# Optimization experiments

Hardware: AMD Instinct MI355X
Metric: run time of the kernel (lower is better)

The kernel has to match this reference:

```python
import jax, jax.numpy as jnp
import numpy as np

N, E = 50000, 400000
EMB, IN, HID, HEADS = 128, 128, 128, 3
RRELU_SLOPE = (1.0 / 8.0 + 1.0 / 3.0) / 2.0  # torch.rrelu eval-mode slope


def _gat_conv(h_in, src, dst, W, a_src, a_dst, b, concat):
    """PyG-style GATConv. h_in: [N, F_in]; src/dst: [E'] (self-loops included)."""
    n = h_in.shape[0]
    h = (h_in @ W).reshape(n, HEADS, -1)            # [N, H, C]
    e_src = jnp.sum(h * a_src, axis=-1)             # [N, H]
    e_dst = jnp.sum(h * a_dst, axis=-1)             # [N, H]
    e = jax.nn.leaky_relu(e_src[src] + e_dst[dst], 0.2)  # [E', H]
    # softmax over incoming edges of each target node
    m = jax.ops.segment_max(e, dst, num_segments=n)
    ex = jnp.exp(e - m[dst])
    denom = jax.ops.segment_sum(ex, dst, num_segments=n)
    alpha = ex / denom[dst]                          # [E', H]
    out = jax.ops.segment_sum(h[src] * alpha[:, :, None], dst, num_segments=n)  # [N,H,C]
    out = out.reshape(n, -1) if concat else out.mean(axis=1)
    return out + b


def _rrelu(x):
    return jnp.where(x >= 0, x, x * RRELU_SLOPE)


def setup_inputs() -> dict:
    key = jax.random.key(0)
    ks = jax.random.split(key, 16)
    d_in = IN + EMB

    def glorot(k, shape):
        fan = sum(shape)
        return jax.random.normal(k, shape, jnp.float32) * np.sqrt(2.0 / fan)

    return {
        "z": jax.random.normal(ks[0], (N, EMB), jnp.float32),
        "x": jax.random.normal(ks[1], (N, IN), jnp.float32),
        "ei": jax.random.randint(ks[2], (2, E), 0, N, jnp.int32),
        "W1": glorot(ks[3], (d_in, HEADS * HID)),
        "a1_src": glorot(ks[4], (HEADS, HID)),
        "a1_dst": glorot(ks[5], (HEADS, HID)),
        "b1": jnp.zeros((HID,), jnp.float32),                 # concat=False -> size C
        "W2": glorot(ks[6], (HID, HEADS * HID)),
        "a2_src": glorot(ks[7], (HEADS, HID)),
        "a2_dst": glorot(ks[8], (HEADS, HID)),
        "b2": jnp.zeros((HEADS * HID,), jnp.float32),         # concat=True -> size H*C
        "W_lin": glorot(ks[9], (HEADS * HID, 1)),
        "b_lin": jnp.zeros((1,), jnp.float32),
    }


def reference(z, x, ei, W1, a1_src, a1_dst, b1, W2, a2_src, a2_dst, b2, W_lin, b_lin):
    n = x.shape[0]
    loops = jnp.arange(n, dtype=ei.dtype)
    src = jnp.concatenate([ei[0], loops])  # PyG add_self_loops=True
    dst = jnp.concatenate([ei[1], loops])
    h = jnp.concatenate([z, x], axis=1)
    h = _rrelu(_gat_conv(h, src, dst, W1, a1_src, a1_dst, b1, concat=False))
    h = _rrelu(_gat_conv(h, src, dst, W2, a2_src, a2_dst, b2, concat=True))
    return jax.nn.sigmoid(h @ W_lin + b_lin)
```

## Files before the change

kernel.cpp:

```cpp
#include <hip/hip_runtime.h>
#include <stdint.h>

#define HEADS 3
#define HID 128
#define FDIM (HEADS * HID)

typedef __attribute__((ext_vector_type(8))) short bf16x8;
typedef __attribute__((ext_vector_type(4))) float f32x4;

__device__ __forceinline__ float lrelu(float x) { return x >= 0.f ? x : 0.2f * x; }
__device__ __forceinline__ float rrelu(float x) {
    const float SLOPE = (1.0f / 8.0f + 1.0f / 3.0f) * 0.5f;
    return x >= 0.f ? x : SLOPE * x;
}
__device__ __forceinline__ unsigned short f2bf(float f) {
    union { float f; unsigned u; } c; c.f = f;
    unsigned r = c.u + 0x7FFF + ((c.u >> 16) & 1);
    return (unsigned short)(r >> 16);
}
__device__ __forceinline__ float bflo(unsigned u) {
    union { unsigned u; float f; } c; c.u = u << 16; return c.f;
}
__device__ __forceinline__ float bfhi(unsigned u) {
    union { unsigned u; float f; } c; c.u = u & 0xffff0000u; return c.f;
}

__device__ __forceinline__ void gload_lds16(const void* g, void* l) {
    __builtin_amdgcn_global_load_lds(
        (const __attribute__((address_space(1))) void*)g,
        (__attribute__((address_space(3))) void*)l, 16, 0, 0);
}


__global__ void k_hist(const int* __restrict__ dst, int E, int* __restrict__ cnt) {
    for (int i = blockIdx.x * blockDim.x + threadIdx.x; i < E; i += gridDim.x * blockDim.x)
        atomicAdd(&cnt[dst[i]], 1);
}

#define SC_T 256
#define SC_E 8
#define SC_CHUNK (SC_T * SC_E)

__global__ __launch_bounds__(SC_T) void k_scan1(const int* __restrict__ cnt,
                                                int* __restrict__ exc,
                                                int* __restrict__ bsum, int n) {
    __shared__ int sm[SC_T];
    int b = blockIdx.x, t = threadIdx.x;
    int base = b * SC_CHUNK + t * SC_E;
    int v[SC_E];
    int s = 0;
#pragma unroll
    for (int i = 0; i < SC_E; i++) {
        int idx = base + i;
        v[i] = (idx < n) ? cnt[idx] : 0;
        s += v[i];
    }
    sm[t] = s;
    __syncthreads();
    for (int off = 1; off < SC_T; off <<= 1) {
        int x = (t >= off) ? sm[t - off] : 0;
        __syncthreads();
        sm[t] += x;
        __syncthreads();
    }
    int run = sm[t] - s;
    if (t == SC_T - 1) bsum[b] = sm[t];
#pragma unroll
    for (int i = 0; i < SC_E; i++) {
        int idx = base + i;
        if (idx < n) exc[idx] = run;
        run += v[i];
    }
}

__global__ __launch_bounds__(256) void k_scan2(const int* __restrict__ bsum,
                                               int* __restrict__ bpre, int nb) {
    __shared__ int sm[256];
    int t = threadIdx.x;
    int v = (t < nb) ? bsum[t] : 0;
    sm[t] = v;
    __syncthreads();
    for (int off = 1; off < 256; off <<= 1) {
        int x = (t >= off) ? sm[t - off] : 0;
        __syncthreads();
        sm[t] += x;
        __syncthreads();
    }
    if (t < nb) bpre[t + 1] = sm[t];
    if (t == 0) bpre[0] = 0;
}

__global__ void k_scan3(int* __restrict__ offs, const int* __restrict__ bpre,
                        int* __restrict__ cursor, int n, int nb) {
    int i = blockIdx.x * blockDim.x + threadIdx.x;
    if (i < n) {
        int o = offs[i] + bpre[i / SC_CHUNK];
        offs[i] = o;
        cursor[i] = o;
    }
    if (i == 0) offs[n] = bpre[nb];
}

__global__ void k_scatter(const int* __restrict__ src, const int* __restrict__ dst, int E,
                          int* __restrict__ cursor, int* __restrict__ ssrc,
                          int* __restrict__ sdst) {
    for (int i = blockIdx.x * blockDim.x + threadIdx.x; i < E; i += gridDim.x * blockDim.x) {
        int d = dst[i];
        int p = atomicAdd(&cursor[d], 1);
        ssrc[p] = src[i];
        sdst[p] = d;
    }
}


__global__ void k_cvt_wt(const float* __restrict__ W, unsigned short* __restrict__ WT,
                         int K, int Ncols) {
    int n = blockIdx.x;
    for (int k = threadIdx.x; k < K; k += blockDim.x)
        WT[(size_t)n * K + k] = f2bf(W[(size_t)k * Ncols + n]);
}


template <bool F32A>
__global__ __launch_bounds__(256) void k_gemm(
    const void* __restrict__ Ap0, const void* __restrict__ Ap1, int Nn,
    const unsigned short* __restrict__ BT,
    unsigned short* __restrict__ C,
    int K, int Ncols,
    const float* __restrict__ asrc, const float* __restrict__ adst,
    float* __restrict__ es, float* __restrict__ ed, int Nnodes) {
    __shared__ __align__(16) unsigned short As[64 * 32];
    __shared__ __align__(16) unsigned short Bs[128 * 32];
    __shared__ float esP[64][2], edP[64][2];
    int tid = threadIdx.x;
    int w = tid >> 6, lane = tid & 63;
    int row0 = blockIdx.x * 64;
    int head = blockIdx.y;
    int col0 = head * 128;
    int wr = w >> 1, wc = w & 1;

    f32x4 acc[2][4] = {};
    int frow = lane & 15;
    int fk = (lane >> 4) * 8;

    const float* zf = (const float*)Ap0;
    const float* xf = (const float*)Ap1;
    float4 va[2];
    if (F32A) {
#pragma unroll
        for (int i = 0; i < 2; i++) {
            int idx = i * 256 + tid;
            int row = idx >> 3, c4 = (idx & 7) * 4;
            int gr = row0 + row;
            const float* sp = zf + (size_t)gr * 128 + c4;
            va[i] = (gr < Nn) ? *(const float4*)sp : make_float4(0.f, 0.f, 0.f, 0.f);
        }
    }

    for (int k0 = 0; k0 < K; k0 += 32) {
#pragma unroll
        for (int i = 0; i < 2; i++) {
            int c = (i * 4 + w) * 64 + lane;
            gload_lds16(BT + (size_t)(col0 + (c >> 2)) * K + k0 + (c & 3) * 8,
                        (char*)Bs + (i * 4 + w) * 1024);
        }
        if (F32A) {
#pragma unroll
            for (int i = 0; i < 2; i++) {
                int idx = i * 256 + tid;
                unsigned short o[4] = {f2bf(va[i].x), f2bf(va[i].y),
                                       f2bf(va[i].z), f2bf(va[i].w)};
                *(uint2*)((char*)As + (size_t)idx * 8) = *(uint2*)o;
            }
        } else {
            const unsigned short* A = (const unsigned short*)Ap0;
            int c = tid;
            gload_lds16(A + (size_t)(row0 + (c >> 2)) * K + k0 + (c & 3) * 8,
                        (char*)As + w * 1024);
        }
        asm volatile("s_waitcnt vmcnt(0)" ::: "memory");
        __syncthreads();

        if (F32A && (k0 + 32 < K)) {
            int kn = k0 + 32;
#pragma unroll
            for (int i = 0; i < 2; i++) {
                int idx = i * 256 + tid;
                int row = idx >> 3, c4 = (idx & 7) * 4;
                int gr = row0 + row;
                const float* sp = (kn < 128)
                                      ? (zf + (size_t)gr * 128 + kn + c4)
                                      : (xf + (size_t)gr * 128 + (kn - 128) + c4);
                va[i] = (gr < Nn) ? *(const float4*)sp : make_float4(0.f, 0.f, 0.f, 0.f);
            }
        }

        bf16x8 af[2], bfr[4];
#pragma unroll
        for (int m = 0; m < 2; m++)
            af[m] = *(const bf16x8*)&As[(wr * 32 + m * 16 + frow) * 32 + fk];
#pragma unroll
        for (int n = 0; n < 4; n++)
            bfr[n] = *(const bf16x8*)&Bs[(wc * 64 + n * 16 + frow) * 32 + fk];
#pragma unroll
        for (int m = 0; m < 2; m++)
#pragma unroll
            for (int n = 0; n < 4; n++)
                acc[m][n] = __builtin_amdgcn_mfma_f32_16x16x32_bf16(af[m], bfr[n], acc[m][n], 0, 0, 0);
        __syncthreads();
    }

    int ccol = lane & 15, crow = (lane >> 4) * 4;

#pragma unroll
    for (int m = 0; m < 2; m++)
#pragma unroll
        for (int n = 0; n < 4; n++)
#pragma unroll
            for (int j = 0; j < 4; j++) {
                int r = row0 + wr * 32 + m * 16 + crow + j;
                int cc = col0 + wc * 64 + n * 16 + ccol;
                C[(size_t)r * Ncols + cc] = f2bf(acc[m][n][j]);
            }

    float as4[4], ad4[4];
#pragma unroll
    for (int n = 0; n < 4; n++) {
        int col_sub = wc * 64 + n * 16 + ccol;
        as4[n] = asrc[head * HID + col_sub];
        ad4[n] = adst[head * HID + col_sub];
    }
#pragma unroll
    for (int m = 0; m < 2; m++)
#pragma unroll
        for (int j = 0; j < 4; j++) {
            float ps = 0.f, pd = 0.f;
#pragma unroll
            for (int n = 0; n < 4; n++) {
                float v = acc[m][n][j];
                ps = fmaf(v, as4[n], ps);
                pd = fmaf(v, ad4[n], pd);
            }
#pragma unroll
            for (int off = 1; off < 16; off <<= 1) {
                ps += __shfl_xor(ps, off);
                pd += __shfl_xor(pd, off);
            }
            if (ccol == 0) {
                int row_sub = wr * 32 + m * 16 + crow + j;
                esP[row_sub][wc] = ps;
                edP[row_sub][wc] = pd;
            }
        }
    __syncthreads();
    if (tid < 64) {
        int r = row0 + tid;
        if (r < Nnodes) {
            es[(size_t)r * 4 + head] = esP[tid][0] + esP[tid][1];
            ed[(size_t)r * 4 + head] = edP[tid][0] + edP[tid][1];
        }
    }
}


__global__ void k_edge_w(const int* __restrict__ ssrc, const int* __restrict__ sdst,
                         const float* __restrict__ es, const float* __restrict__ ed,
                         float4* __restrict__ w4, int E) {
    for (int j = blockIdx.x * blockDim.x + threadIdx.x; j < E; j += gridDim.x * blockDim.x) {
        int s = ssrc[j], d = sdst[j];
        float4 a = *(const float4*)&es[(size_t)s * 4];
        float4 b = *(const float4*)&ed[(size_t)d * 4];
        float w0 = __expf(lrelu(a.x + b.x));
        float w1 = __expf(lrelu(a.y + b.y));
        float w2 = __expf(lrelu(a.z + b.z));
        w4[j] = make_float4(w0, w1, w2, 0.f);
    }
}


#define EDGE_UNROLL4(body)                                                       \
    int j = j0;                                                                  \
    for (; j + 4 <= j1; j += 4) {                                                \
        int si[4]; float4 wv[4]; unsigned uu[4][3];                              \
        _Pragma("unroll") for (int e = 0; e < 4; e++) si[e] = ssrc[j + e];       \
        _Pragma("unroll") for (int e = 0; e < 4; e++) wv[e] = w4[j + e];         \
        _Pragma("unroll") for (int e = 0; e < 4; e++) {                          \
            const unsigned* rp = Hu + (size_t)si[e] * 192 + L;                   \
            uu[e][0] = rp[0]; uu[e][1] = rp[64]; uu[e][2] = rp[128];             \
        }                                                                        \
        _Pragma("unroll") for (int e = 0; e < 4; e++) { body(wv[e], uu[e]) }     \
    }                                                                            \
    for (; j < j1; j++) {                                                        \
        int s1_ = ssrc[j]; float4 w_ = w4[j];                                    \
        const unsigned* rp = Hu + (size_t)s1_ * 192 + L;                         \
        unsigned u_[3] = {rp[0], rp[64], rp[128]};                               \
        { body(w_, u_) }                                                         \
    }

#define ACC3(wv, uv)                                                             \
    a0[0] = fmaf(wv.x, bflo(uv[0]), a0[0]); a1[0] = fmaf(wv.x, bfhi(uv[0]), a1[0]); \
    a0[1] = fmaf(wv.y, bflo(uv[1]), a0[1]); a1[1] = fmaf(wv.y, bfhi(uv[1]), a1[1]); \
    a0[2] = fmaf(wv.z, bflo(uv[2]), a0[2]); a1[2] = fmaf(wv.z, bfhi(uv[2]), a1[2]); \
    den0 += wv.x; den1 += wv.y; den2 += wv.z;

__global__ __launch_bounds__(256) void k_agg_mean(const unsigned* __restrict__ Hu,
                                                  const float4* __restrict__ w4,
                                                  const float* __restrict__ es,
                                                  const float* __restrict__ ed,
                                                  const int* __restrict__ offs,
                                                  const int* __restrict__ ssrc,
                                                  const float* __restrict__ b,
                                                  unsigned* __restrict__ out, int Nn) {
    int L = threadIdx.x & 63;
    int wstep = gridDim.x * 4;
    for (int n = blockIdx.x * 4 + (threadIdx.x >> 6); n < Nn; n += wstep) {
        float4 esn = *(const float4*)&es[(size_t)n * 4];
        float4 edn = *(const float4*)&ed[(size_t)n * 4];
        float s0 = __expf(lrelu(esn.x + edn.x));
        float s1 = __expf(lrelu(esn.y + edn.y));
        float s2 = __expf(lrelu(esn.z + edn.z));
        float den0 = s0, den1 = s1, den2 = s2;
        const unsigned* rp = Hu + (size_t)n * 192 + L;
        unsigned u0 = rp[0], u1 = rp[64], u2 = rp[128];
        float a0[3] = {s0 * bflo(u0), s1 * bflo(u1), s2 * bflo(u2)};
        float a1[3] = {s0 * bfhi(u0), s1 * bfhi(u1), s2 * bfhi(u2)};
        int j0 = offs[n], j1 = offs[n + 1];
        EDGE_UNROLL4(ACC3)
        float iv0 = 1.f / den0, iv1 = 1.f / den1, iv2 = 1.f / den2;
        int c0 = 2 * L;
        float2 bb = *(const float2*)&b[c0];
        float m0 = (a0[0] * iv0 + a0[1] * iv1 + a0[2] * iv2) * (1.f / 3.f) + bb.x;
        float m1 = (a1[0] * iv0 + a1[1] * iv1 + a1[2] * iv2) * (1.f / 3.f) + bb.y;
        unsigned short o[2] = {f2bf(rrelu(m0)), f2bf(rrelu(m1))};
        out[(size_t)n * 64 + L] = *(unsigned*)o;
    }
}

__global__ __launch_bounds__(256) void k_agg_cat_final(const unsigned* __restrict__ Hu,
                                                       const float4* __restrict__ w4,
                                                       const float* __restrict__ es,
                                                       const float* __restrict__ ed,
                                                       const int* __restrict__ offs,
                                                       const int* __restrict__ ssrc,
                                                       const float* __restrict__ b,
                                                       const float* __restrict__ Wl,
                                                       const float* __restrict__ bl,
                                                       float* __restrict__ out, int Nn) {
    int L = threadIdx.x & 63;
    int wstep = gridDim.x * 4;
    for (int n = blockIdx.x * 4 + (threadIdx.x >> 6); n < Nn; n += wstep) {
        float4 esn = *(const float4*)&es[(size_t)n * 4];
        float4 edn = *(const float4*)&ed[(size_t)n * 4];
        float s0 = __expf(lrelu(esn.x + edn.x));
        float s1 = __expf(lrelu(esn.y + edn.y));
        float s2 = __expf(lrelu(esn.z + edn.z));
        float den0 = s0, den1 = s1, den2 = s2;
        const unsigned* rp = Hu + (size_t)n * 192 + L;
        unsigned u0 = rp[0], u1 = rp[64], u2 = rp[128];
        float a0[3] = {s0 * bflo(u0), s1 * bflo(u1), s2 * bflo(u2)};
        float a1[3] = {s0 * bfhi(u0), s1 * bfhi(u1), s2 * bfhi(u2)};
        int j0 = offs[n], j1 = offs[n + 1];
        EDGE_UNROLL4(ACC3)
        float ivv[3] = {1.f / den0, 1.f / den1, 1.f / den2};
        float p = 0.f;
#pragma unroll
        for (int k = 0; k < 3; k++) {
            int col = k * HID + 2 * L;
            float2 bb = *(const float2*)&b[col];
            float2 wl = *(const float2*)&Wl[col];
            float r0 = rrelu(a0[k] * ivv[k] + bb.x);
            float r1 = rrelu(a1[k] * ivv[k] + bb.y);
            p = fmaf(r0, wl.x, p);
            p = fmaf(r1, wl.y, p);
        }
#pragma unroll
        for (int off = 32; off > 0; off >>= 1) p += __shfl_down(p, off);
        if (L == 0) out[n] = 1.f / (1.f + __expf(-(p + bl[0])));
    }
}


extern "C" void kernel_launch(void* const* d_in, const int* in_sizes, int n_in,
                              void* d_out, int out_size, void* d_ws, size_t ws_size,
                              hipStream_t stream) {
    const float* z   = (const float*)d_in[0];
    const float* x   = (const float*)d_in[1];
    const int*   ei  = (const int*)d_in[2];
    const float* W1  = (const float*)d_in[3];
    const float* a1s = (const float*)d_in[4];
    const float* a1d = (const float*)d_in[5];
    const float* b1  = (const float*)d_in[6];
    const float* W2  = (const float*)d_in[7];
    const float* a2s = (const float*)d_in[8];
    const float* a2d = (const float*)d_in[9];
    const float* b2  = (const float*)d_in[10];
    const float* Wl  = (const float*)d_in[11];
    const float* bl  = (const float*)d_in[12];
    float* outp = (float*)d_out;

    int Nn = in_sizes[0] / 128;
    int E  = in_sizes[2] / 2;
    int Mpad = (Nn + 127) & ~127;
    int nb = (Nn + SC_CHUNK - 1) / SC_CHUNK;

    char* p = (char*)d_ws;
    auto carve = [&](size_t bytes) -> char* {
        char* r = p;
        p += (bytes + 255) & ~(size_t)255;
        return r;
    };
    int*            offs   = (int*)carve((size_t)(Nn + 1) * 4);
    int*            cursor = (int*)carve((size_t)Nn * 4);
    int*            ssrc   = (int*)carve((size_t)E * 4);
    int*            sdst   = (int*)carve((size_t)E * 4);
    int*            bsum   = (int*)carve((size_t)(nb + 1) * 4);
    int*            bpre   = (int*)carve((size_t)(nb + 1) * 4);
    float*          e1s    = (float*)carve((size_t)Mpad * 16);
    float*          e1d    = (float*)carve((size_t)Mpad * 16);
    float4*         w4     = (float4*)carve((size_t)E * 16);
    unsigned short* W1T    = (unsigned short*)carve((size_t)FDIM * 256 * 2);
    unsigned short* W2T    = (unsigned short*)carve((size_t)FDIM * 128 * 2);
    unsigned short* Hbf    = (unsigned short*)carve((size_t)Mpad * FDIM * 2);
    unsigned short* H2in   = (unsigned short*)carve((size_t)Mpad * 128 * 2);

    const int* srcI = ei;
    const int* dstI = ei + E;

    hipMemsetAsync(cursor, 0, (size_t)Nn * 4, stream);
    k_hist<<<1024, 256, 0, stream>>>(dstI, E, cursor);
    k_scan1<<<nb, SC_T, 0, stream>>>(cursor, offs, bsum, Nn);
    k_scan2<<<1, 256, 0, stream>>>(bsum, bpre, nb);
    k_scan3<<<(Nn + 255) / 256, 256, 0, stream>>>(offs, bpre, cursor, Nn, nb);
    k_scatter<<<1024, 256, 0, stream>>>(srcI, dstI, E, cursor, ssrc, sdst);

    k_cvt_wt<<<FDIM, 256, 0, stream>>>(W1, W1T, 256, FDIM);
    k_cvt_wt<<<FDIM, 128, 0, stream>>>(W2, W2T, 128, FDIM);
    hipMemsetAsync(H2in + (size_t)Nn * 128, 0, (size_t)(Mpad - Nn) * 128 * 2, stream);

    dim3 gg(Mpad / 64, FDIM / 128);

    k_gemm<true><<<gg, 256, 0, stream>>>(z, x, Nn, W1T, Hbf, 256, FDIM,
                                         a1s, a1d, e1s, e1d, Nn);
    k_edge_w<<<1024, 256, 0, stream>>>(ssrc, sdst, e1s, e1d, w4, E);
    k_agg_mean<<<2048, 256, 0, stream>>>((const unsigned*)Hbf, w4, e1s, e1d, offs,
                                         ssrc, b1, (unsigned*)H2in, Nn);

    k_gemm<false><<<gg, 256, 0, stream>>>(H2in, nullptr, Mpad, W2T, Hbf, 128, FDIM,
                                          a2s, a2d, e1s, e1d, Nn);
    k_edge_w<<<1024, 256, 0, stream>>>(ssrc, sdst, e1s, e1d, w4, E);
    k_agg_cat_final<<<2048, 256, 0, stream>>>((const unsigned*)Hbf, w4, e1s, e1d, offs,
                                              ssrc, b2, Wl, bl, outp, Nn);
}
```

Baseline: 250.3 us.

## Keep full A row-tile in LDS and loop all heads per block with double-buffered B

The GEMM now loads the whole 64-row A tile, converting it to bf16 and padding its rows, into LDS once, then loops over all three heads inside one block instead of launching one block per head. Re-reading and re-converting the fp32 z/x inputs three times is avoided. B tiles are double-buffered so the next slice's load overlaps current MFMA work, and the two weight-transpose launches are merged into one. In exchange, LDS use per block grows (about 34KB for K=256), the grid shrinks threefold, and each block runs a longer serial loop, which may lower occupancy and parallelism.

```diff
diff --git a/kernel.cpp b/kernel.cpp
--- a/kernel.cpp
+++ b/kernel.cpp
@@ -113,11 +113,17 @@
 }
 
 
-__global__ void k_cvt_wt(const float* __restrict__ W, unsigned short* __restrict__ WT,
-                         int K, int Ncols) {
-    int n = blockIdx.x;
-    for (int k = threadIdx.x; k < K; k += blockDim.x)
-        WT[(size_t)n * K + k] = f2bf(W[(size_t)k * Ncols + n]);
+__global__ void k_cvt_wt2(const float* __restrict__ W1, unsigned short* __restrict__ W1T,
+                          const float* __restrict__ W2, unsigned short* __restrict__ W2T) {
+    int b = blockIdx.x;
+    if (b < FDIM) {
+        for (int k = threadIdx.x; k < 256; k += blockDim.x)
+            W1T[(size_t)b * 256 + k] = f2bf(W1[(size_t)k * FDIM + b]);
+    } else {
+        int n = b - FDIM;
+        for (int k = threadIdx.x; k < 128; k += blockDim.x)
+            W2T[(size_t)n * 128 + k] = f2bf(W2[(size_t)k * FDIM + n]);
+    }
 }
 
 
@@ -129,137 +135,151 @@
     int K, int Ncols,
     const float* __restrict__ asrc, const float* __restrict__ adst,
     float* __restrict__ es, float* __restrict__ ed, int Nnodes) {
-    __shared__ __align__(16) unsigned short As[64 * 32];
-    __shared__ __align__(16) unsigned short Bs[128 * 32];
+    __shared__ __align__(16) unsigned short As[64 * 264];
+    __shared__ __align__(16) unsigned short Bs[2][128 * 32];
     __shared__ float esP[64][2], edP[64][2];
     int tid = threadIdx.x;
     int w = tid >> 6, lane = tid & 63;
     int row0 = blockIdx.x * 64;
-    int head = blockIdx.y;
-    int col0 = head * 128;
     int wr = w >> 1, wc = w & 1;
-
-    f32x4 acc[2][4] = {};
+    int KP = K + 8;
+    int KS = K >> 5;
+
     int frow = lane & 15;
     int fk = (lane >> 4) * 8;
 
-    const float* zf = (const float*)Ap0;
-    const float* xf = (const float*)Ap1;
-    float4 va[2];
     if (F32A) {
-#pragma unroll
-        for (int i = 0; i < 2; i++) {
+        const float* zf = (const float*)Ap0;
+        const float* xf = (const float*)Ap1;
+#pragma unroll 8
+        for (int i = 0; i < 16; i++) {
             int idx = i * 256 + tid;
-            int row = idx >> 3, c4 = (idx & 7) * 4;
+            int row = idx >> 6;
+            int c4 = (idx & 63) * 4;
             int gr = row0 + row;
-            const float* sp = zf + (size_t)gr * 128 + c4;
-            va[i] = (gr < Nn) ? *(const float4*)sp : make_float4(0.f, 0.f, 0.f, 0.f);
+            float4 v = make_float4(0.f, 0.f, 0.f, 0.f);
+            if (gr < Nn) {
+                const float* sp = (c4 < 128) ? zf + (size_t)gr * 128 + c4
+                                             : xf + (size_t)gr * 128 + (c4 - 128);
+                v = *(const float4*)sp;
+            }
+            unsigned short o[4] = {f2bf(v.x), f2bf(v.y), f2bf(v.z), f2bf(v.w)};
+            *(uint2*)&As[row * KP + c4] = *(uint2*)o;
         }
-    }
-
-    for (int k0 = 0; k0 < K; k0 += 32) {
-#pragma unroll
-        for (int i = 0; i < 2; i++) {
-            int c = (i * 4 + w) * 64 + lane;
-            gload_lds16(BT + (size_t)(col0 + (c >> 2)) * K + k0 + (c & 3) * 8,
-                        (char*)Bs + (i * 4 + w) * 1024);
+    } else {
+        const unsigned short* A = (const unsigned short*)Ap0;
+        int cpr = K >> 3;
+#pragma unroll 4
+        for (int i = 0; i < 4; i++) {
+            int idx = i * 256 + tid;
+            int row = idx / cpr;
+            int c8 = (idx - row * cpr) * 8;
+            uint4 v = *(const uint4*)&A[(size_t)(row0 + row) * K + c8];
+            *(uint4*)&As[row * KP + c8] = v;
         }
-        if (F32A) {
-#pragma unroll
-            for (int i = 0; i < 2; i++) {
-                int idx = i * 256 + tid;
-                unsigned short o[4] = {f2bf(va[i].x), f2bf(va[i].y),
-                                       f2bf(va[i].z), f2bf(va[i].w)};
-                *(uint2*)((char*)As + (size_t)idx * 8) = *(uint2*)o;
-            }
-        } else {
-            const unsigned short* A = (const unsigned short*)Ap0;
-            int c = tid;
-            gload_lds16(A + (size_t)(row0 + (c >> 2)) * K + k0 + (c & 3) * 8,
-                        (char*)As + w * 1024);
-        }
+    }
+
+#define STAGE_B(hh, kk, buf)                                                      \
+    {                                                                             \
+        int k0s = (kk) << 5;                                                      \
+        _Pragma("unroll") for (int i = 0; i < 2; i++) {                           \
+            int c = (i * 4 + w) * 64 + lane;                                      \
+            gload_lds16(BT + (size_t)((hh) * 128 + (c >> 2)) * K + k0s + (c & 3) * 8, \
+                        (char*)Bs[buf] + (i * 4 + w) * 1024);                     \
+        }                                                                         \
+    }
+
+    STAGE_B(0, 0, 0)
+
+    f32x4 acc[2][4] = {};
+    int cur = 0;
+    int h = 0, ks = 0;
+    int total = 3 * KS;
+    for (int it = 0; it < total; ++it) {
         asm volatile("s_waitcnt vmcnt(0)" ::: "memory");
         __syncthreads();
 
-        if (F32A && (k0 + 32 < K)) {
-            int kn = k0 + 32;
-#pragma unroll
-            for (int i = 0; i < 2; i++) {
-                int idx = i * 256 + tid;
-                int row = idx >> 3, c4 = (idx & 7) * 4;
-                int gr = row0 + row;
-                const float* sp = (kn < 128)
-                                      ? (zf + (size_t)gr * 128 + kn + c4)
-                                      : (xf + (size_t)gr * 128 + (kn - 128) + c4);
-                va[i] = (gr < Nn) ? *(const float4*)sp : make_float4(0.f, 0.f, 0.f, 0.f);
-            }
-        }
-
+        int nh = h, nks = ks + 1;
+        if (nks == KS) { nh = h + 1; nks = 0; }
+        if (nh < 3) STAGE_B(nh, nks, cur ^ 1)
+
+        int k0 = ks << 5;
         bf16x8 af[2], bfr[4];
 #pragma unroll
         for (int m = 0; m < 2; m++)
-            af[m] = *(const bf16x8*)&As[(wr * 32 + m * 16 + frow) * 32 + fk];
+            af[m] = *(const bf16x8*)&As[(wr * 32 + m * 16 + frow) * KP + k0 + fk];
 #pragma unroll
         for (int n = 0; n < 4; n++)
-            bfr[n] = *(const bf16x8*)&Bs[(wc * 64 + n * 16 + frow) * 32 + fk];
+            bfr[n] = *(const bf16x8*)&Bs[cur][(wc * 64 + n * 16 + frow) * 32 + fk];
 #pragma unroll
         for (int m = 0; m < 2; m++)
 #pragma unroll
             for (int n = 0; n < 4; n++)
                 acc[m][n] = __builtin_amdgcn_mfma_f32_16x16x32_bf16(af[m], bfr[n], acc[m][n], 0, 0, 0);
-        __syncthreads();
-    }
-
-    int ccol = lane & 15, crow = (lane >> 4) * 4;
-
-#pragma unroll
-    for (int m = 0; m < 2; m++)
-#pragma unroll
-        for (int n = 0; n < 4; n++)
-#pragma unroll
-            for (int j = 0; j < 4; j++) {
-                int r = row0 + wr * 32 + m * 16 + crow + j;
-                int cc = col0 + wc * 64 + n * 16 + ccol;
-                C[(size_t)r * Ncols + cc] = f2bf(acc[m][n][j]);
+
+        if (ks == KS - 1) {
+            int ccol = lane & 15, crow = (lane >> 4) * 4;
+            int col0 = h * 128;
+#pragma unroll
+            for (int m = 0; m < 2; m++)
+#pragma unroll
+                for (int n = 0; n < 4; n++)
+#pragma unroll
+                    for (int j = 0; j < 4; j++) {
+                        int r = row0 + wr * 32 + m * 16 + crow + j;
+                        int cc = col0 + wc * 64 + n * 16 + ccol;
+                        C[(size_t)r * Ncols + cc] = f2bf(acc[m][n][j]);
+                    }
+            float as4[4], ad4[4];
+#pragma unroll
+            for (int n = 0; n < 4; n++) {
+                int col_sub = wc * 64 + n * 16 + ccol;
+                as4[n] = asrc[h * HID + col_sub];
+                ad4[n] = adst[h * HID + col_sub];
             }
-
-    float as4[4], ad4[4];
-#pragma unroll
-    for (int n = 0; n < 4; n++) {
-        int col_sub = wc * 64 + n * 16 + ccol;
-        as4[n] = asrc[head * HID + col_sub];
-        ad4[n] = adst[head * HID + col_sub];
-    }
-#pragma unroll
-    for (int m = 0; m < 2; m++)
-#pragma unroll
-        for (int j = 0; j < 4; j++) {
-            float ps = 0.f, pd = 0.f;
-#pragma unroll
-            for (int n = 0; n < 4; n++) {
-                float v = acc[m][n][j];
-                ps = fmaf(v, as4[n], ps);
-                pd = fmaf(v, ad4[n], pd);
+#pragma unroll
+            for (int m = 0; m < 2; m++)
+#pragma unroll
+                for (int j = 0; j < 4; j++) {
+                    float ps = 0.f, pd = 0.f;
+#pragma unroll
+                    for (int n = 0; n < 4; n++) {
+                        float v = acc[m][n][j];
+                        ps = fmaf(v, as4[n], ps);
+                        pd = fmaf(v, ad4[n], pd);
+                    }
+#pragma unroll
+                    for (int off = 1; off < 16; off <<= 1) {
+                        ps += __shfl_xor(ps, off);
+                        pd += __shfl_xor(pd, off);
+                    }
+                    if (ccol == 0) {
+                        int row_sub = wr * 32 + m * 16 + crow + j;
+                        esP[row_sub][wc] = ps;
+                        edP[row_sub][wc] = pd;
+                    }
+                }
+            __syncthreads();
+            if (tid < 64) {
+                int r = row0 + tid;
+                if (r < Nnodes) {
+                    es[(size_t)r * 4 + h] = esP[tid][0] + esP[tid][1];
+                    ed[(size_t)r * 4 + h] = edP[tid][0] + edP[tid][1];
+                }
             }
 #pragma unroll
-            for (int off = 1; off < 16; off <<= 1) {
-                ps += __shfl_xor(ps, off);
-                pd += __shfl_xor(pd, off);
-            }
-            if (ccol == 0) {
-                int row_sub = wr * 32 + m * 16 + crow + j;
-                esP[row_sub][wc] = ps;
-                edP[row_sub][wc] = pd;
-            }
+            for (int m = 0; m < 2; m++)
+#pragma unroll
+                for (int n = 0; n < 4; n++)
+                    acc[m][n] = f32x4{0.f, 0.f, 0.f, 0.f};
+            h++;
+            ks = 0;
+        } else {
+            ks++;
         }
-    __syncthreads();
-    if (tid < 64) {
-        int r = row0 + tid;
-        if (r < Nnodes) {
-            es[(size_t)r * 4 + head] = esP[tid][0] + esP[tid][1];
-            ed[(size_t)r * 4 + head] = edP[tid][0] + edP[tid][1];
-        }
-    }
+        cur ^= 1;
+    }
+#undef STAGE_B
 }
 
 
@@ -433,11 +453,10 @@
     k_scan3<<<(Nn + 255) / 256, 256, 0, stream>>>(offs, bpre, cursor, Nn, nb);
     k_scatter<<<1024, 256, 0, stream>>>(srcI, dstI, E, cursor, ssrc, sdst);
 
-    k_cvt_wt<<<FDIM, 256, 0, stream>>>(W1, W1T, 256, FDIM);
-    k_cvt_wt<<<FDIM, 128, 0, stream>>>(W2, W2T, 128, FDIM);
+    k_cvt_wt2<<<2 * FDIM, 256, 0, stream>>>(W1, W1T, W2, W2T);
     hipMemsetAsync(H2in + (size_t)Nn * 128, 0, (size_t)(Mpad - Nn) * 128 * 2, stream);
 
-    dim3 gg(Mpad / 64, FDIM / 128);
+    int gg = Mpad / 64;
 
     k_gemm<true><<<gg, 256, 0, stream>>>(z, x, Nn, W1T, Hbf, 256, FDIM,
                                          a1s, a1d, e1s, e1d, Nn);
```

After: 276.7 us. 10.5% more time.
